# Optimization experiments

Measured on AMD Instinct MI355X. Metric: run time of the kernel, lower is better.

The kernel has to match this reference:

```python
import jax, jax.numpy as jnp
import numpy as np

EPS = 0.01       # l2-normalize epsilon
BN_EPS = 0.001   # batchnorm epsilon

def _l2norm(u):
    # tf.math.l2_normalize over axis=-2: x / sqrt(max(sum(x^2), eps))
    sq = jnp.sum(u * u, axis=-2, keepdims=True)
    return u / jnp.sqrt(jnp.maximum(sq, EPS))

def _dotprod(t, u):
    # einsum '...ij,...ik->...jk' contracting spatial axis, then flatten (C,C)->C*C
    d = jnp.einsum('bndi,bndj->bnij', t, _l2norm(u))
    return d.reshape(d.shape[0], d.shape[1], -1)

def _bn(x, gamma, beta):
    # inference-mode BN with moving_mean=0, moving_var=1 (fresh init)
    return gamma * (x / jnp.sqrt(1.0 + BN_EPS)) + beta

def setup_inputs() -> dict:
    key = jax.random.key(0)
    ks = jax.random.split(key, 9)
    B, N, D, C, BAS, U_IN, U_EQ = 8, 1024, 3, 64, 16, 512, 64
    F = 2 * C * C  # 8192 invariant features (2 input heads)
    t1 = jax.random.normal(ks[0], (B, N, D, C), dtype=jnp.float32)
    t2 = jax.random.normal(ks[1], (B, N, D, C), dtype=jnp.float32)
    u1 = jax.random.normal(ks[2], (B, N, D, C), dtype=jnp.float32)
    u2 = jax.random.normal(ks[3], (B, N, D, C), dtype=jnp.float32)
    V1 = jax.random.normal(ks[4], (B, N, D, BAS), dtype=jnp.float32)
    V2 = jax.random.normal(ks[5], (B, N, D, BAS), dtype=jnp.float32)
    W_inv = jax.random.normal(ks[6], (F, U_IN), dtype=jnp.float32) * 0.02
    b_inv = jnp.zeros((U_IN,), dtype=jnp.float32)
    g_inv = jnp.ones((U_IN,), dtype=jnp.float32)
    be_inv = jnp.zeros((U_IN,), dtype=jnp.float32)
    # two equivariant heads, each Dense(units=U_EQ*BAS)
    W_eq = jax.random.normal(ks[7], (2, F, U_EQ * BAS), dtype=jnp.float32) * 0.02
    b_eq = jnp.zeros((2, U_EQ * BAS), dtype=jnp.float32)
    g_eq = jnp.ones((2, U_EQ * BAS), dtype=jnp.float32)
    be_eq = jnp.zeros((2, U_EQ * BAS), dtype=jnp.float32)
    return {"t1": t1, "t2": t2, "u1": u1, "u2": u2, "V1": V1, "V2": V2,
            "W_inv": W_inv, "b_inv": b_inv, "g_inv": g_inv, "be_inv": be_inv,
            "W_eq": W_eq, "b_eq": b_eq, "g_eq": g_eq, "be_eq": be_eq}

def reference(t1, t2, u1, u2, V1, V2, W_inv, b_inv, g_inv, be_inv,
              W_eq, b_eq, g_eq, be_eq):
    # invariant features: concatenated flattened Gram blocks of the two heads
    feats = jnp.concatenate([_dotprod(t1, u1), _dotprod(t2, u2)], axis=-1)  # (B,N,F)
    # invariant branch: Dense -> BN -> ReLU
    invar = jax.nn.relu(_bn(feats @ W_inv + b_inv, g_inv, be_inv))  # (B,N,U_IN)
    # equivariant branch per head: Dense -> BN -> ReLU -> reshape -> basis recombine
    bas = V1.shape[-1]
    u_eq = W_eq.shape[-1] // bas
    eq_outs = []
    for l, V in enumerate((V1, V2)):
        wl = jax.nn.relu(_bn(feats @ W_eq[l] + b_eq[l], g_eq[l], be_eq[l]))
        wl = wl.reshape(wl.shape[0], wl.shape[1], u_eq, bas)  # (B,N,units,basis)
        # einsum '...ij,...mj->...mi': combine basis vectors -> (B,N,3,units)
        eq_outs.append(jnp.einsum('bnij,bnmj->bnmi', wl, V))
    eqvar = jnp.concatenate(eq_outs, axis=-1)  # (B,N,3,2*units)
    return invar, eqvar
```

## Files before the change

kernel.cpp:

```cpp
#include <hip/hip_runtime.h>
#include <hip/hip_bf16.h>

#define BROWS 8192
#define DDIM 3
#define CDIM 64
#define KF 8192
#define NINV 512
#define NEQ 1024
#define NTOT 2560
#define BAS 16
#define UEQ 64


typedef float f32x4 __attribute__((ext_vector_type(4)));
typedef __bf16 bf16x8_t __attribute__((ext_vector_type(8)));
typedef __bf16 bf16x4_t __attribute__((ext_vector_type(4)));

__device__ __forceinline__ void async_copy16(const void* g, void* l) {
    __builtin_amdgcn_global_load_lds(
        (__attribute__((address_space(1))) void*)(g),
        (__attribute__((address_space(3))) void*)(l), 16, 0, 0);
}

__global__ __launch_bounds__(256) void feats_kernel(
    const float* __restrict__ t1, const float* __restrict__ t2,
    const float* __restrict__ u1, const float* __restrict__ u2,
    __hip_bfloat16* __restrict__ feats)
{
    const int row = blockIdx.x;
    const int tid = threadIdx.x;
    __shared__ float sT[2 * DDIM * CDIM];
    __shared__ float sU[2 * DDIM * CDIM];

    const size_t base = (size_t)row * (DDIM * CDIM);
    if (tid < 192) {
        sT[tid]       = t1[base + tid];
        sT[192 + tid] = t2[base + tid];
        sU[tid]       = u1[base + tid];
        sU[192 + tid] = u2[base + tid];
    }
    __syncthreads();
    if (tid < 128) {
        const int h = tid >> 6, c = tid & 63;
        float* U = sU + h * 192;
        float sq = U[c] * U[c] + U[64 + c] * U[64 + c] + U[128 + c] * U[128 + c];
        float s = 1.0f / sqrtf(fmaxf(sq, 0.01f));
        U[c] *= s; U[64 + c] *= s; U[128 + c] *= s;
    }
    __syncthreads();
    const int h  = tid >> 7;
    const int i  = (tid >> 1) & 63;
    const int jh = (tid & 1) * 32;
    const float* T = sT + h * 192;
    const float* U = sU + h * 192;
    const float ti0 = T[i], ti1 = T[64 + i], ti2 = T[128 + i];

    const int kbase = h * 4096 + i * 64 + jh;
    const int kt    = kbase >> 5;
    const int mb    = row >> 8, rloc = row & 255;
    char* line = (char*)feats + (((size_t)(mb * 256 + kt)) << 14) + rloc * 64;

    #pragma unroll
    for (int g = 0; g < 4; ++g) {
        const int phys = (g + (rloc >> 1)) & 3;
        #pragma unroll
        for (int half = 0; half < 2; ++half) {
            const int j = jh + g * 8 + half * 4;
            const float4 u0 = *reinterpret_cast<const float4*>(U + j);
            const float4 u1 = *reinterpret_cast<const float4*>(U + 64 + j);
            const float4 u2 = *reinterpret_cast<const float4*>(U + 128 + j);
            bf16x4_t v;
            v[0] = (__bf16)(ti0 * u0.x + ti1 * u1.x + ti2 * u2.x);
            v[1] = (__bf16)(ti0 * u0.y + ti1 * u1.y + ti2 * u2.y);
            v[2] = (__bf16)(ti0 * u0.z + ti1 * u1.z + ti2 * u2.z);
            v[3] = (__bf16)(ti0 * u0.w + ti1 * u1.w + ti2 * u2.w);
            *reinterpret_cast<bf16x4_t*>(line + phys * 16 + half * 8) = v;
        }
    }
}

__global__ __launch_bounds__(256) void wt_kernel(
    const float* __restrict__ W_inv, const float* __restrict__ W_eq,
    __hip_bfloat16* __restrict__ WT)
{
    __shared__ float tile[32][33];
    const int tid = threadIdx.x;
    const int tx = tid & 31;
    const int ty = tid >> 5;
    const int n0 = blockIdx.x * 32;
    const int k0 = blockIdx.y * 32;

    const float* src; int ldn, nl0;
    if (n0 < NINV)            { src = W_inv;                       ldn = NINV; nl0 = n0; }
    else if (n0 < NINV + NEQ) { src = W_eq;                        ldn = NEQ;  nl0 = n0 - NINV; }
    else                      { src = W_eq + (size_t)KF * NEQ;     ldn = NEQ;  nl0 = n0 - NINV - NEQ; }

    #pragma unroll
    for (int i = 0; i < 4; ++i) {
        int kl = ty + i * 8;
        tile[kl][tx] = src[(size_t)(k0 + kl) * ldn + nl0 + tx];
    }
    __syncthreads();
    const int n_l = tid >> 3;
    const int k4  = (tid & 7) * 4;
    bf16x4_t v;
    #pragma unroll
    for (int q = 0; q < 4; ++q) v[q] = (__bf16)tile[k4 + q][n_l];

    const int n    = n0 + n_l;
    const int nb   = n / 320, rloc = n - nb * 320;
    const int kt   = k0 >> 5;
    const int lc   = (k4 >> 3) & 3, e = k4 & 7;
    const int phys = (lc + (rloc >> 1)) & 3;
    char* dst = (char*)WT + ((size_t)(nb * 256 + kt)) * 20480
              + rloc * 64 + phys * 16 + e * 2;
    *reinterpret_cast<bf16x4_t*>(dst) = v;
}

#define BM 256
#define BN 320
#define BK 32
#define ATILE 16384
#define BTILE 20480

__global__ __launch_bounds__(512, 2) void gemm_kernel(
    const __hip_bfloat16* __restrict__ A,
    const __hip_bfloat16* __restrict__ BT,
    const float* __restrict__ b_inv, const float* __restrict__ g_inv,
    const float* __restrict__ be_inv,
    const float* __restrict__ b_eq,  const float* __restrict__ g_eq,
    const float* __restrict__ be_eq,
    float* __restrict__ out_inv,
    float* __restrict__ Yeq)
{
    __shared__ alignas(16) __hip_bfloat16 AsBuf[4][BM * BK];
    __shared__ alignas(16) __hip_bfloat16 BsBuf[4][BN * BK];

    const int tid  = threadIdx.x;
    const int wave = tid >> 6;
    const int lane = tid & 63;
    const bool aWave = wave < 4;

    const int b    = blockIdx.x;
    const int xcd  = b & 7;
    const int slot = b >> 3;
    const int nb   = slot & 7;
    const int mb   = xcd * 4 + (slot >> 3);
    const int n0   = nb * BN;
    const int m0   = mb * BM;

    const char* pA = (const char*)A  + ((size_t)mb << 22);
    const char* pB = (const char*)BT + (size_t)nb * 256 * BTILE;

    const int aoff = wave * 4096 + lane * 16;
    const int boff = (wave - 4) * 5120 + lane * 16;

    const int chnk = (((lane >> 4) + ((lane & 15) >> 1)) & 3) * 8;
    const int wm = (wave & 3) * 64;
    const int wn = (wave >> 2) * 160;
    const int l15 = lane & 15;

    f32x4 acc[4][10] = {};

#define ISSUE(bufi, t)                                                        \
    do {                                                                      \
        if (aWave) {                                                          \
            _Pragma("unroll")                                                 \
            for (int j = 0; j < 4; ++j)                                       \
                async_copy16(pA + (size_t)(t) * ATILE + aoff + j * 1024,      \
                             (char*)&AsBuf[bufi][0] + aoff + j * 1024);       \
        } else {                                                              \
            _Pragma("unroll")                                                 \
            for (int j = 0; j < 5; ++j)                                       \
                async_copy16(pB + (size_t)(t) * BTILE + boff + j * 1024,      \
                             (char*)&BsBuf[bufi][0] + boff + j * 1024);       \
        }                                                                     \
    } while (0)

#define COMPUTE(bufi)                                                         \
    do {                                                                      \
        bf16x8_t a_[4];                                                       \
        _Pragma("unroll")                                                     \
        for (int mt = 0; mt < 4; ++mt)                                        \
            a_[mt] = *reinterpret_cast<const bf16x8_t*>(                      \
                &AsBuf[bufi][(wm + mt * 16 + l15) * BK + chnk]);              \
        _Pragma("unroll")                                                     \
        for (int nt = 0; nt < 10; ++nt) {                                     \
            bf16x8_t b_ = *reinterpret_cast<const bf16x8_t*>(                 \
                &BsBuf[bufi][(wn + nt * 16 + l15) * BK + chnk]);              \
            _Pragma("unroll")                                                 \
            for (int mt = 0; mt < 4; ++mt)                                    \
                acc[mt][nt] = __builtin_amdgcn_mfma_f32_16x16x32_bf16(        \
                    a_[mt], b_, acc[mt][nt], 0, 0, 0);                        \
        }                                                                     \
    } while (0)

#define WAITAB(na, nb_)                                                       \
    do {                                                                      \
        if (aWave) asm volatile("s_waitcnt vmcnt(" #na ")" ::: "memory");     \
        else       asm volatile("s_waitcnt vmcnt(" #nb_ ")" ::: "memory");    \
    } while (0)

#define MPHASE(b0, b1, t)                                                     \
    do {                                                                      \
        WAITAB(8, 10);                                                        \
        __builtin_amdgcn_s_barrier();                                         \
        asm volatile("" ::: "memory");                                        \
        COMPUTE(b0);                                                          \
        asm volatile("" ::: "memory");                                        \
        COMPUTE(b1);                                                          \
        asm volatile("" ::: "memory");                                        \
        __builtin_amdgcn_s_barrier();                                         \
        ISSUE(b0, t + 4);                                                     \
        ISSUE(b1, t + 5);                                                     \
    } while (0)

    ISSUE(0, 0);
    ISSUE(1, 1);
    ISSUE(2, 2);
    ISSUE(3, 3);

    for (int i = 0; i < 63; ++i) {
        const int t = i * 4;
        MPHASE(0, 1, t);
        MPHASE(2, 3, t + 2);
    }
    WAITAB(8, 10);
    __builtin_amdgcn_s_barrier();
    asm volatile("" ::: "memory");
    COMPUTE(0);
    asm volatile("" ::: "memory");
    COMPUTE(1);
    asm volatile("" ::: "memory");
    __builtin_amdgcn_s_barrier();

    asm volatile("s_waitcnt vmcnt(0)" ::: "memory");
    __builtin_amdgcn_s_barrier();
    asm volatile("" ::: "memory");
    COMPUTE(2);
    asm volatile("" ::: "memory");
    COMPUTE(3);

    const float RSQ = 0.9995003746877732f;
    #pragma unroll
    for (int nt = 0; nt < 10; ++nt) {
        const int gn = n0 + wn + nt * 16 + l15;
        float bbp, gg, bep;
        if (gn < NINV) {
            bbp = b_inv[gn]; gg = g_inv[gn]; bep = be_inv[gn];
        } else {
            const int e = gn - NINV, hh = e >> 10, nl = e & 1023;
            bbp = b_eq[hh * NEQ + nl]; gg = g_eq[hh * NEQ + nl]; bep = be_eq[hh * NEQ + nl];
        }
        gg *= RSQ;
        #pragma unroll
        for (int mt = 0; mt < 4; ++mt) {
            const int gmb = m0 + wm + mt * 16 + ((lane >> 4) << 2);
            #pragma unroll
            for (int rr = 0; rr < 4; ++rr) {
                float y = fmaxf(gg * (acc[mt][nt][rr] + bbp) + bep, 0.0f);
                const size_t gm = gmb + rr;
                if (gn < NINV) out_inv[gm * NINV + gn] = y;
                else           Yeq[gm * 2048 + (gn - NINV)] = y;
            }
        }
    }
#undef MPHASE
#undef WAITAB
#undef COMPUTE
#undef ISSUE
}

__global__ __launch_bounds__(128) void eqcomb_kernel(
    const float* __restrict__ Yeq,
    const float* __restrict__ V1, const float* __restrict__ V2,
    float* __restrict__ out_eq)
{
    const int row = blockIdx.x;
    const int tid = threadIdx.x;
    __shared__ float sV[2][DDIM][BAS];
    if (tid < 96) {
        const int h = tid / 48, rem = tid % 48;
        const float* V = h ? V2 : V1;
        sV[h][rem / BAS][rem % BAS] = V[(size_t)row * (DDIM * BAS) + rem];
    }
    __syncthreads();
    const int l = tid >> 6, u = tid & 63;
    const float4* y4 = reinterpret_cast<const float4*>(
        Yeq + (size_t)row * 2048 + l * 1024 + u * BAS);
    float a0 = 0.f, a1 = 0.f, a2 = 0.f;
    #pragma unroll
    for (int q = 0; q < 4; ++q) {
        float4 w = y4[q];
        const float* v0 = sV[l][0] + q * 4;
        const float* v1 = sV[l][1] + q * 4;
        const float* v2 = sV[l][2] + q * 4;
        a0 += w.x * v0[0] + w.y * v0[1] + w.z * v0[2] + w.w * v0[3];
        a1 += w.x * v1[0] + w.y * v1[1] + w.z * v1[2] + w.w * v1[3];
        a2 += w.x * v2[0] + w.y * v2[1] + w.z * v2[2] + w.w * v2[3];
    }
    float* o = out_eq + (size_t)row * (DDIM * 128);
    o[0 * 128 + l * 64 + u] = a0;
    o[1 * 128 + l * 64 + u] = a1;
    o[2 * 128 + l * 64 + u] = a2;
}

extern "C" void kernel_launch(void* const* d_in, const int* in_sizes, int n_in,
                              void* d_out, int out_size, void* d_ws, size_t ws_size,
                              hipStream_t stream) {
    const float* t1    = (const float*)d_in[0];
    const float* t2    = (const float*)d_in[1];
    const float* u1    = (const float*)d_in[2];
    const float* u2    = (const float*)d_in[3];
    const float* V1    = (const float*)d_in[4];
    const float* V2    = (const float*)d_in[5];
    const float* W_inv = (const float*)d_in[6];
    const float* b_inv = (const float*)d_in[7];
    const float* g_inv = (const float*)d_in[8];
    const float* be_inv= (const float*)d_in[9];
    const float* W_eq  = (const float*)d_in[10];
    const float* b_eq  = (const float*)d_in[11];
    const float* g_eq  = (const float*)d_in[12];
    const float* be_eq = (const float*)d_in[13];
    float* out = (float*)d_out;

    char* ws = (char*)d_ws;
    __hip_bfloat16* feats = (__hip_bfloat16*)(ws);
    __hip_bfloat16* WT    = (__hip_bfloat16*)(ws + 134217728);
    float*          Yeq   = (float*)(ws + 176160768);

    float* out_inv = out;
    float* out_eq  = out + (size_t)BROWS * NINV;

    hipLaunchKernelGGL(feats_kernel, dim3(BROWS), dim3(256), 0, stream,
                       t1, t2, u1, u2, feats);
    hipLaunchKernelGGL(wt_kernel, dim3(NTOT / 32, KF / 32), dim3(256), 0, stream,
                       W_inv, W_eq, WT);
    hipLaunchKernelGGL(gemm_kernel, dim3((NTOT / BN) * (BROWS / BM)), dim3(512), 0, stream,
                       feats, WT, b_inv, g_inv, be_inv, b_eq, g_eq, be_eq,
                       out_inv, Yeq);
    hipLaunchKernelGGL(eqcomb_kernel, dim3(BROWS), dim3(128), 0, stream,
                       Yeq, V1, V2, out_eq);
}
```

Measured before the change: 582.6 us.

## Process 16 rows per block in feats kernel with coalesced 16-byte stores

The feature-building kernel now handles 16 rows per block instead of one, staging the inputs in padded shared memory. Each wavefront writes whole contiguous 1 KB segments of the tiled bf16 feature layout with 16-byte stores, where before each thread issued scattered 8-byte stores. The goal is better write coalescing and less per-block overhead on the feature matrix, which is about 128 MB. The cost is more shared memory per block and a different thread-to-output mapping, which must keep the swizzle exactly consistent.

```diff
diff --git a/kernel.cpp b/kernel.cpp
--- a/kernel.cpp
+++ b/kernel.cpp
@@ -22,60 +22,82 @@
         (__attribute__((address_space(3))) void*)(l), 16, 0, 0);
 }
 
+#define FROWS 16
+#define FSTRIDE 196
+
 __global__ __launch_bounds__(256) void feats_kernel(
     const float* __restrict__ t1, const float* __restrict__ t2,
     const float* __restrict__ u1, const float* __restrict__ u2,
     __hip_bfloat16* __restrict__ feats)
 {
-    const int row = blockIdx.x;
+    __shared__ float sT1[FROWS * FSTRIDE];
+    __shared__ float sT2[FROWS * FSTRIDE];
+    __shared__ float sU1[FROWS * FSTRIDE];
+    __shared__ float sU2[FROWS * FSTRIDE];
+
     const int tid = threadIdx.x;
-    __shared__ float sT[2 * DDIM * CDIM];
-    __shared__ float sU[2 * DDIM * CDIM];
-
-    const size_t base = (size_t)row * (DDIM * CDIM);
-    if (tid < 192) {
-        sT[tid]       = t1[base + tid];
-        sT[192 + tid] = t2[base + tid];
-        sU[tid]       = u1[base + tid];
-        sU[192 + tid] = u2[base + tid];
+    const int r0  = blockIdx.x * FROWS;
+
+    #pragma unroll
+    for (int k = 0; k < 12; ++k) {
+        const int item = k * 256 + tid;
+        const int r = item / 192, c = item - r * 192;
+        const size_t g = (size_t)(r0 + r) * 192 + c;
+        const int l = r * FSTRIDE + c;
+        sT1[l] = t1[g];
+        sT2[l] = t2[g];
+        sU1[l] = u1[g];
+        sU2[l] = u2[g];
     }
     __syncthreads();
-    if (tid < 128) {
-        const int h = tid >> 6, c = tid & 63;
-        float* U = sU + h * 192;
+
+    #pragma unroll
+    for (int k = 0; k < 8; ++k) {
+        const int item = k * 256 + tid;
+        const int r = item >> 7, rem = item & 127;
+        const int h = rem >> 6, c = rem & 63;
+        float* U = (h ? sU2 : sU1) + r * FSTRIDE;
         float sq = U[c] * U[c] + U[64 + c] * U[64 + c] + U[128 + c] * U[128 + c];
         float s = 1.0f / sqrtf(fmaxf(sq, 0.01f));
         U[c] *= s; U[64 + c] *= s; U[128 + c] *= s;
     }
     __syncthreads();
-    const int h  = tid >> 7;
-    const int i  = (tid >> 1) & 63;
-    const int jh = (tid & 1) * 32;
-    const float* T = sT + h * 192;
-    const float* U = sU + h * 192;
-    const float ti0 = T[i], ti1 = T[64 + i], ti2 = T[128 + i];
-
-    const int kbase = h * 4096 + i * 64 + jh;
-    const int kt    = kbase >> 5;
-    const int mb    = row >> 8, rloc = row & 255;
-    char* line = (char*)feats + (((size_t)(mb * 256 + kt)) << 14) + rloc * 64;
-
-    #pragma unroll
-    for (int g = 0; g < 4; ++g) {
-        const int phys = (g + (rloc >> 1)) & 3;
+
+    const int w       = tid >> 6;
+    const int lane    = tid & 63;
+    const int r_local = lane >> 2;
+    const int p       = lane & 3;
+    const int mb      = r0 >> 8;
+    const int rloc0   = r0 & 255;
+    const int rloc    = rloc0 + r_local;
+    const int lc      = (p - (rloc >> 1)) & 3;
+    const float* Tarr = (w >= 2 ? sT2 : sT1) + r_local * FSTRIDE;
+    const float* Uarr = (w >= 2 ? sU2 : sU1) + r_local * FSTRIDE;
+
+    char* dst = (char*)feats + (((size_t)(mb * 256 + w * 64)) << 14)
+              + rloc0 * 64 + lane * 16;
+
+    #pragma unroll 4
+    for (int it = 0; it < 64; ++it) {
+        const int kt = w * 64 + it;
+        const int i  = (kt >> 1) & 63;
+        const int jh = (kt & 1) * 32;
+        const int j0 = jh + lc * 8;
+        const float ti0 = Tarr[i], ti1 = Tarr[64 + i], ti2 = Tarr[128 + i];
+        bf16x8_t vv;
         #pragma unroll
         for (int half = 0; half < 2; ++half) {
-            const int j = jh + g * 8 + half * 4;
-            const float4 u0 = *reinterpret_cast<const float4*>(U + j);
-            const float4 u1 = *reinterpret_cast<const float4*>(U + 64 + j);
-            const float4 u2 = *reinterpret_cast<const float4*>(U + 128 + j);
-            bf16x4_t v;
-            v[0] = (__bf16)(ti0 * u0.x + ti1 * u1.x + ti2 * u2.x);
-            v[1] = (__bf16)(ti0 * u0.y + ti1 * u1.y + ti2 * u2.y);
-            v[2] = (__bf16)(ti0 * u0.z + ti1 * u1.z + ti2 * u2.z);
-            v[3] = (__bf16)(ti0 * u0.w + ti1 * u1.w + ti2 * u2.w);
-            *reinterpret_cast<bf16x4_t*>(line + phys * 16 + half * 8) = v;
+            const int j = j0 + half * 4;
+            const float4 u0 = *reinterpret_cast<const float4*>(Uarr + j);
+            const float4 u1_ = *reinterpret_cast<const float4*>(Uarr + 64 + j);
+            const float4 u2_ = *reinterpret_cast<const float4*>(Uarr + 128 + j);
+            vv[half * 4 + 0] = (__bf16)(ti0 * u0.x + ti1 * u1_.x + ti2 * u2_.x);
+            vv[half * 4 + 1] = (__bf16)(ti0 * u0.y + ti1 * u1_.y + ti2 * u2_.y);
+            vv[half * 4 + 2] = (__bf16)(ti0 * u0.z + ti1 * u1_.z + ti2 * u2_.z);
+            vv[half * 4 + 3] = (__bf16)(ti0 * u0.w + ti1 * u1_.w + ti2 * u2_.w);
         }
+        *reinterpret_cast<bf16x8_t*>(dst) = vv;
+        dst += 16384;
     }
 }
 
@@ -332,7 +354,7 @@
     float* out_inv = out;
     float* out_eq  = out + (size_t)BROWS * NINV;
 
-    hipLaunchKernelGGL(feats_kernel, dim3(BROWS), dim3(256), 0, stream,
+    hipLaunchKernelGGL(feats_kernel, dim3(BROWS / FROWS), dim3(256), 0, stream,
                        t1, t2, u1, u2, feats);
     hipLaunchKernelGGL(wt_kernel, dim3(NTOT / 32, KF / 32), dim3(256), 0, stream,
                        W_inv, W_eq, WT);
```

Result: faster. 546.4 us (-6.2%).
